# Kernel tuning notes

Measured on AMD Instinct MI355X. Metric: run time of the kernel, lower is better.

The kernel has to match this reference:

```python
import jax, jax.numpy as jnp
import numpy as np

EPS = 1e-6
N_HEADS = 16


def _stable_softmax(x):
    # max subtracted with stop_gradient (torch .detach()), clamp to [-50, 50], eps in denom
    x_max = jax.lax.stop_gradient(jnp.max(x, axis=-1, keepdims=True))
    exp_x = jnp.exp(jnp.clip(x - x_max, -50.0, 50.0))
    return exp_x / (jnp.sum(exp_x, axis=-1, keepdims=True) + EPS)


def setup_inputs() -> dict:
    key = jax.random.key(0)
    k1, k2, k3 = jax.random.split(key, 3)
    B, S, D = 2, 2048, 1024
    x = jax.random.normal(k1, (B, S, D), dtype=jnp.float32)
    Wqkv = jax.random.normal(k2, (3 * D, D), dtype=jnp.float32) * 0.02
    Wout = jax.random.normal(k3, (D, D), dtype=jnp.float32) * (0.02 / np.sqrt(2))
    return {"x": x, "Wqkv": Wqkv, "Wout": Wout}


def reference(x, Wqkv, Wout):
    B, S, D = x.shape
    H = N_HEADS
    Dh = D // H
    scale = 1.0 / np.sqrt(Dh)
    # qkv projection (torch Linear: x @ W.T), split into q,k,v -> (B,H,S,Dh)
    qkv = (x @ Wqkv.T).reshape(B, S, 3, H, Dh)
    qkv = jnp.transpose(qkv, (2, 0, 3, 1, 4))
    q, k, v = qkv[0], qkv[1], qkv[2]
    # chunked attention is mathematically identical to full attention here
    scores = jnp.einsum('bhqd,bhkd->bhqk', q, k) * scale
    attn = _stable_softmax(scores)
    out = jnp.einsum('bhqk,bhkd->bhqd', attn, v)  # (B,H,S,Dh)
    out = jnp.transpose(out, (0, 2, 1, 3)).reshape(B, S, D)
    return out @ Wout.T
```

## Files before the change

kernel.cpp:

```cpp
#include <hip/hip_runtime.h>
#include <hip/hip_bf16.h>
#include <stdint.h>

#define S_LEN   2048
#define D_MODEL 1024
#define NH      16
#define DH      64
#define BATCH   2
#define TOKENS  (BATCH * S_LEN)

typedef __bf16 bf16;
typedef __bf16 bf16x8 __attribute__((ext_vector_type(8)));
typedef __bf16 b16x4  __attribute__((ext_vector_type(4)));
typedef float  f32x4  __attribute__((ext_vector_type(4)));
typedef float  f32x16 __attribute__((ext_vector_type(16)));
typedef unsigned int uint32;

__device__ __forceinline__ void async_lds16(const void* g, void* l) {
  __builtin_amdgcn_global_load_lds((__attribute__((address_space(1))) void*)g,
                                   (__attribute__((address_space(3))) void*)l,
                                   16, 0, 0);
}

__global__ __launch_bounds__(256) void convert2_kernel(
    const float* __restrict__ s0, bf16* __restrict__ d0, int n0,
    const float* __restrict__ s1, bf16* __restrict__ d1, int n1) {
  int i = blockIdx.x * 256 + threadIdx.x;
  const float* s;
  bf16* d;
  if (i < n0) {
    s = s0 + (size_t)i * 8; d = d0 + (size_t)i * 8;
  } else {
    i -= n0;
    if (i >= n1) return;
    s = s1 + (size_t)i * 8; d = d1 + (size_t)i * 8;
  }
  const f32x4 a = *(const f32x4*)s;
  const f32x4 b = *(const f32x4*)(s + 4);
  bf16x8 o;
#pragma unroll
  for (int j = 0; j < 4; j++) { o[j] = (bf16)a[j]; o[j + 4] = (bf16)b[j]; }
  *(bf16x8*)d = o;
}

#define BM 128
#define BN 128
#define BK 32

#define GEMM_CORE(APTR, BPTR, KDIM)                                              \
  __shared__ __align__(16) bf16 As[BM * BK];                                     \
  __shared__ __align__(16) bf16 Bs[BN * BK];                                     \
  const int tid  = threadIdx.x;                                                  \
  const int wave = tid >> 6, lane = tid & 63;                                    \
  const int quad = lane >> 4, l16 = lane & 15;                                   \
  const int m0 = blockIdx.y * BM;                                                \
  const int n0 = blockIdx.x * BN;                                                \
  const int wm = (wave >> 1) * 64, wn = (wave & 1) * 64;                         \
  f32x4 acc[4][4] = {};                                                          \
  const int c0 = tid, c1 = tid + 256;                                            \
  for (int k0 = 0; k0 < (KDIM); k0 += BK) {                                      \
    async_lds16((APTR) + (size_t)(m0 + (c0 >> 2)) * (KDIM) + k0 + (c0 & 3) * 8,  \
                As + c0 * 8);                                                    \
    async_lds16((APTR) + (size_t)(m0 + (c1 >> 2)) * (KDIM) + k0 + (c1 & 3) * 8,  \
                As + c1 * 8);                                                    \
    async_lds16((BPTR) + (size_t)(n0 + (c0 >> 2)) * (KDIM) + k0 + (c0 & 3) * 8,  \
                Bs + c0 * 8);                                                    \
    async_lds16((BPTR) + (size_t)(n0 + (c1 >> 2)) * (KDIM) + k0 + (c1 & 3) * 8,  \
                Bs + c1 * 8);                                                    \
    __syncthreads();                                                             \
    bf16x8 af[4], bfr[4];                                                        \
    _Pragma("unroll") for (int i = 0; i < 4; i++)                                \
        af[i] = *(const bf16x8*)(As + (wm + i * 16 + l16) * BK + quad * 8);      \
    _Pragma("unroll") for (int j = 0; j < 4; j++)                                \
        bfr[j] = *(const bf16x8*)(Bs + (wn + j * 16 + l16) * BK + quad * 8);     \
    _Pragma("unroll") for (int i = 0; i < 4; i++)                                \
      _Pragma("unroll") for (int j = 0; j < 4; j++)                              \
        acc[i][j] = __builtin_amdgcn_mfma_f32_16x16x32_bf16(af[i], bfr[j],       \
                                                            acc[i][j], 0, 0, 0); \
    __syncthreads();                                                             \
  }

__global__ __launch_bounds__(256) void gemm_qkv_kernel(
    const bf16* __restrict__ X, const bf16* __restrict__ W,
    bf16* __restrict__ Qo, bf16* __restrict__ Ko, bf16* __restrict__ VTo) {
  GEMM_CORE(X, W, D_MODEL)
  const int t = n0 >> 10;
#pragma unroll
  for (int i = 0; i < 4; i++) {
    const int rowb = m0 + wm + i * 16 + quad * 4;
    const int b = rowb >> 11, s0 = rowb & 2047;
#pragma unroll
    for (int j = 0; j < 4; j++) {
      const int col = n0 + wn + j * 16 + l16;
      const int h = (col >> 6) & 15, d = col & 63;
      if (t == 2) {
        b16x4 v4;
#pragma unroll
        for (int r = 0; r < 4; r++) v4[r] = (bf16)acc[i][j][r];
        *(b16x4*)(VTo + ((size_t)(b * NH + h) * DH + d) * S_LEN + s0) = v4;
      } else {
#pragma unroll
        for (int r = 0; r < 4; r++) {
          const float v = acc[i][j][r];
          if (t == 0)
            Qo[((size_t)(b * NH + h) * S_LEN + s0 + r) * DH + d] = (bf16)(v * 0.125f);
          else
            Ko[((size_t)(b * NH + h) * S_LEN + s0 + r) * DH + d] = (bf16)v;
        }
      }
    }
  }
}

#define BM2 64
#define BN2 128

__global__ __launch_bounds__(256) void gemm_out_kernel(
    const bf16* __restrict__ A, const bf16* __restrict__ W,
    float* __restrict__ Out) {
  __shared__ __align__(16) bf16 As[BM2 * BK];
  __shared__ __align__(16) bf16 Bs[BN2 * BK];
  const int tid  = threadIdx.x;
  const int wave = tid >> 6, lane = tid & 63;
  const int quad = lane >> 4, l16 = lane & 15;
  const int m0 = blockIdx.y * BM2;
  const int n0 = blockIdx.x * BN2;
  const int wm = (wave >> 1) * 32, wn = (wave & 1) * 64;
  f32x4 acc[2][4] = {};
  const int c0 = tid, c1 = tid + 256;
  for (int k0 = 0; k0 < D_MODEL; k0 += BK) {
    async_lds16(A + (size_t)(m0 + (c0 >> 2)) * D_MODEL + k0 + (c0 & 3) * 8,
                As + c0 * 8);
    async_lds16(W + (size_t)(n0 + (c0 >> 2)) * D_MODEL + k0 + (c0 & 3) * 8,
                Bs + c0 * 8);
    async_lds16(W + (size_t)(n0 + (c1 >> 2)) * D_MODEL + k0 + (c1 & 3) * 8,
                Bs + c1 * 8);
    __syncthreads();
    bf16x8 af[2], bfr[4];
#pragma unroll
    for (int i = 0; i < 2; i++)
      af[i] = *(const bf16x8*)(As + (wm + i * 16 + l16) * BK + quad * 8);
#pragma unroll
    for (int j = 0; j < 4; j++)
      bfr[j] = *(const bf16x8*)(Bs + (wn + j * 16 + l16) * BK + quad * 8);
#pragma unroll
    for (int i = 0; i < 2; i++)
#pragma unroll
      for (int j = 0; j < 4; j++)
        acc[i][j] = __builtin_amdgcn_mfma_f32_16x16x32_bf16(af[i], bfr[j],
                                                            acc[i][j], 0, 0, 0);
    __syncthreads();
  }
#pragma unroll
  for (int i = 0; i < 2; i++) {
    const int rowb = m0 + wm + i * 16 + quad * 4;
#pragma unroll
    for (int j = 0; j < 4; j++) {
      const int col = n0 + wn + j * 16 + l16;
#pragma unroll
      for (int r = 0; r < 4; r++)
        Out[(size_t)(rowb + r) * D_MODEL + col] = acc[i][j][r];
    }
  }
}

__global__ __launch_bounds__(512, 2) void attn_kernel(
    const bf16* __restrict__ Q, const bf16* __restrict__ K,
    const bf16* __restrict__ VT, bf16* __restrict__ AO) {
  __shared__ __align__(16) bf16 smem[2][2][2 * 64 * 64];

  const int tid  = threadIdx.x;
  const int lane = tid & 63;
  const int wave = tid >> 6;
  const int g    = wave >> 2;
  const int qw   = wave & 3;
  const int l31  = lane & 31;
  const int hi   = lane >> 5;
  const int sw   = l31 & 7;

  const int bid = (blockIdx.x & 7) * 32 + (blockIdx.x >> 3);
  const int qb  = bid & 7;
  const int bh  = bid >> 3;

  const bf16* qp = Q  + ((size_t)bh * S_LEN + qb * 256 + qw * 64 + l31) * DH;
  const bf16* kp = K  + (size_t)bh * S_LEN * DH;
  const bf16* vp = VT + (size_t)bh * DH * S_LEN;

  bf16x8 qf0[4], qf1[4];
#pragma unroll
  for (int dk = 0; dk < 4; dk++) {
    qf0[dk] = *(const bf16x8*)(qp + dk * 16 + hi * 8);
    qf1[dk] = *(const bf16x8*)(qp + 32 * DH + dk * 16 + hi * 8);
  }

  const int gtid = tid & 255;
  const int cid0 = gtid, cid1 = gtid + 256;
  const int r0 = cid0 >> 3, c0 = (cid0 & 7) ^ (r0 & 7);
  const int r1 = cid1 >> 3, c1 = (cid1 & 7) ^ (r1 & 7);
  const bf16* ka0 = kp + (size_t)(g * 64 + r0) * DH + c0 * 8;
  const bf16* ka1 = kp + (size_t)(g * 64 + r1) * DH + c1 * 8;
  const bf16* va0 = vp + (size_t)r0 * S_LEN + g * 64 + c0 * 8;
  const bf16* va1 = vp + (size_t)r1 * S_LEN + g * 64 + c1 * 8;
  const int ld0 = cid0 * 8, ld1 = cid1 * 8;

  f32x16 oT0[2] = {}, oT1[2] = {};
  float lsum0 = 0.f, lsum1 = 0.f;

  bf16* sg = &smem[g][0][0];

#define STAGE(B)                                                                 \
  {                                                                              \
    bf16* s = sg + (B) * (2 * 64 * 64);                                          \
    async_lds16(ka0, s + ld0);                                                   \
    async_lds16(ka1, s + ld1);                                                   \
    async_lds16(va0, s + 4096 + ld0);                                            \
    async_lds16(va1, s + 4096 + ld1);                                            \
    ka0 += 8192; ka1 += 8192; va0 += 128; va1 += 128;                            \
  }

  STAGE(0)

#pragma unroll 2
  for (int t = 0; t < 16; t++) {
    const int cur = t & 1;
    asm volatile("s_waitcnt vmcnt(0)" ::: "memory");
    __builtin_amdgcn_s_barrier();
    if (t < 15) {
      STAGE(cur ^ 1)
    }

    const bf16* sb = sg + cur * (2 * 64 * 64);

    bf16x8 vfr[8];
#pragma unroll
    for (int dt = 0; dt < 2; dt++)
#pragma unroll
      for (int ks = 0; ks < 4; ks++)
        vfr[dt * 4 + ks] = *(const bf16x8*)(sb + 4096 + (dt * 32 + l31) * 64 +
                                            (((ks * 2 + hi) ^ sw) * 8));

    f32x16 st0[2] = {}, st1[2] = {};
    __builtin_amdgcn_s_setprio(1);
#pragma unroll
    for (int kt = 0; kt < 2; kt++)
#pragma unroll
      for (int dk = 0; dk < 4; dk++) {
        const bf16x8 kf = *(const bf16x8*)(sb + (kt * 32 + l31) * 64 +
                                           (((dk * 2 + hi) ^ sw) * 8));
        st0[kt] = __builtin_amdgcn_mfma_f32_32x32x16_bf16(kf, qf0[dk], st0[kt], 0, 0, 0);
        st1[kt] = __builtin_amdgcn_mfma_f32_32x32x16_bf16(kf, qf1[dk], st1[kt], 0, 0, 0);
      }
    __builtin_amdgcn_s_setprio(0);

#pragma unroll
    for (int kt = 0; kt < 2; kt++)
#pragma unroll
      for (int hk = 0; hk < 2; hk++) {
        const int ks = kt * 2 + hk;
        float e0[8], e1[8];
#pragma unroll
        for (int r = 0; r < 8; r++) e0[r] = __expf(st0[kt][hk * 8 + r]);
#pragma unroll
        for (int r = 0; r < 8; r++) e1[r] = __expf(st1[kt][hk * 8 + r]);
        lsum0 += ((e0[0] + e0[1]) + (e0[2] + e0[3])) + ((e0[4] + e0[5]) + (e0[6] + e0[7]));
        lsum1 += ((e1[0] + e1[1]) + (e1[2] + e1[3])) + ((e1[4] + e1[5]) + (e1[6] + e1[7]));
        uint32 p00, p01, p02, p03, p10, p11, p12, p13;
        asm("v_cvt_pk_bf16_f32 %0, %1, %2" : "=v"(p00) : "v"(e0[0]), "v"(e0[1]));
        asm("v_cvt_pk_bf16_f32 %0, %1, %2" : "=v"(p01) : "v"(e0[2]), "v"(e0[3]));
        asm("v_cvt_pk_bf16_f32 %0, %1, %2" : "=v"(p02) : "v"(e0[4]), "v"(e0[5]));
        asm("v_cvt_pk_bf16_f32 %0, %1, %2" : "=v"(p03) : "v"(e0[6]), "v"(e0[7]));
        asm("v_cvt_pk_bf16_f32 %0, %1, %2" : "=v"(p10) : "v"(e1[0]), "v"(e1[1]));
        asm("v_cvt_pk_bf16_f32 %0, %1, %2" : "=v"(p11) : "v"(e1[2]), "v"(e1[3]));
        asm("v_cvt_pk_bf16_f32 %0, %1, %2" : "=v"(p12) : "v"(e1[4]), "v"(e1[5]));
        asm("v_cvt_pk_bf16_f32 %0, %1, %2" : "=v"(p13) : "v"(e1[6]), "v"(e1[7]));
        asm("v_permlane32_swap_b32 %0, %1" : "+v"(p00), "+v"(p02));
        asm("v_permlane32_swap_b32 %0, %1" : "+v"(p01), "+v"(p03));
        asm("v_permlane32_swap_b32 %0, %1" : "+v"(p10), "+v"(p12));
        asm("v_permlane32_swap_b32 %0, %1" : "+v"(p11), "+v"(p13));
        union { uint32 u[4]; bf16x8 v; } pf0, pf1;
        pf0.u[0] = p00; pf0.u[1] = p01; pf0.u[2] = p02; pf0.u[3] = p03;
        pf1.u[0] = p10; pf1.u[1] = p11; pf1.u[2] = p12; pf1.u[3] = p13;
        __builtin_amdgcn_s_setprio(1);
#pragma unroll
        for (int dt = 0; dt < 2; dt++) {
          oT0[dt] = __builtin_amdgcn_mfma_f32_32x32x16_bf16(vfr[dt * 4 + ks], pf0.v,
                                                            oT0[dt], 0, 0, 0);
          oT1[dt] = __builtin_amdgcn_mfma_f32_32x32x16_bf16(vfr[dt * 4 + ks], pf1.v,
                                                            oT1[dt], 0, 0, 0);
        }
        __builtin_amdgcn_s_setprio(0);
      }
  }
#undef STAGE

  __syncthreads();

  lsum0 += __shfl_xor(lsum0, 32);
  lsum1 += __shfl_xor(lsum1, 32);

  float* mO = (float*)&smem[0][0][0];
  float* mL = mO + 256 * 32;
  const int mrow = qw * 64 + lane;

  if (g == 1) {
#pragma unroll
    for (int j = 0; j < 8; j++) {
      const int dt = j >> 2, rb = (j & 3) * 4;
      f32x4 c = { oT0[dt][rb], oT0[dt][rb + 1], oT0[dt][rb + 2], oT0[dt][rb + 3] };
      *(f32x4*)((char*)mO + mrow * 128 + ((j ^ (lane & 7)) * 16)) = c;
    }
    mL[mrow] = lsum0;
  }
  __syncthreads();
  if (g == 0) {
#pragma unroll
    for (int j = 0; j < 8; j++) {
      const int dt = j >> 2, rb = (j & 3) * 4;
      const f32x4 c = *(const f32x4*)((char*)mO + mrow * 128 + ((j ^ (lane & 7)) * 16));
#pragma unroll
      for (int rr = 0; rr < 4; rr++) oT0[dt][rb + rr] += c[rr];
    }
    lsum0 += mL[mrow];
  }
  __syncthreads();
  if (g == 1) {
#pragma unroll
    for (int j = 0; j < 8; j++) {
      const int dt = j >> 2, rb = (j & 3) * 4;
      f32x4 c = { oT1[dt][rb], oT1[dt][rb + 1], oT1[dt][rb + 2], oT1[dt][rb + 3] };
      *(f32x4*)((char*)mO + mrow * 128 + ((j ^ (lane & 7)) * 16)) = c;
    }
    mL[mrow] = lsum1;
  }
  __syncthreads();
  if (g == 0) {
#pragma unroll
    for (int j = 0; j < 8; j++) {
      const int dt = j >> 2, rb = (j & 3) * 4;
      const f32x4 c = *(const f32x4*)((char*)mO + mrow * 128 + ((j ^ (lane & 7)) * 16));
#pragma unroll
      for (int rr = 0; rr < 4; rr++) oT1[dt][rb + rr] += c[rr];
    }
    lsum1 += mL[mrow];

    const float inv0 = 1.0f / (lsum0 + 1e-6f);
    const float inv1 = 1.0f / (lsum1 + 1e-6f);
    const int b = bh >> 4, h = bh & 15;
    const int srow = qb * 256 + qw * 64 + l31;
    const size_t base0 = (size_t)(b * S_LEN + srow) * D_MODEL + h * DH;
    const size_t base1 = base0 + (size_t)32 * D_MODEL;
#pragma unroll
    for (int dt = 0; dt < 2; dt++)
#pragma unroll
      for (int rg = 0; rg < 4; rg++) {
        b16x4 o4;
#pragma unroll
        for (int rr = 0; rr < 4; rr++) o4[rr] = (bf16)(oT0[dt][rg * 4 + rr] * inv0);
        *(b16x4*)(AO + base0 + dt * 32 + rg * 8 + hi * 4) = o4;
      }
#pragma unroll
    for (int dt = 0; dt < 2; dt++)
#pragma unroll
      for (int rg = 0; rg < 4; rg++) {
        b16x4 o4;
#pragma unroll
        for (int rr = 0; rr < 4; rr++) o4[rr] = (bf16)(oT1[dt][rg * 4 + rr] * inv1);
        *(b16x4*)(AO + base1 + dt * 32 + rg * 8 + hi * 4) = o4;
      }
  }
}

extern "C" void kernel_launch(void* const* d_in, const int* in_sizes, int n_in,
                              void* d_out, int out_size, void* d_ws, size_t ws_size,
                              hipStream_t stream) {
  const float* x    = (const float*)d_in[0];
  const float* wqkv = (const float*)d_in[1];
  const float* wout = (const float*)d_in[2];
  float* out = (float*)d_out;

  bf16* Q  = (bf16*)d_ws;
  bf16* K  = Q  + (size_t)TOKENS * D_MODEL;
  bf16* VT = K  + (size_t)TOKENS * D_MODEL;
  bf16* xb = VT + (size_t)TOKENS * D_MODEL;
  bf16* AO = xb;
  bf16* wqkvb = (bf16*)d_out;
  bf16* woutb = Q;

  const int nx = TOKENS * D_MODEL / 8;
  const int nw = 3 * D_MODEL * D_MODEL / 8;
  const int no = D_MODEL * D_MODEL / 8;
  convert2_kernel<<<dim3((nx + nw) / 256), dim3(256), 0, stream>>>(
      x, xb, nx, wqkv, wqkvb, nw);

  gemm_qkv_kernel<<<dim3(3 * D_MODEL / BN, TOKENS / BM), dim3(256), 0, stream>>>(
      xb, wqkvb, Q, K, VT);

  attn_kernel<<<dim3(BATCH * NH * (S_LEN / 256)), dim3(512), 0, stream>>>(Q, K, VT, AO);

  convert2_kernel<<<dim3(no / 256), dim3(256), 0, stream>>>(
      wout, woutb, no, wout, woutb, 0);

  gemm_out_kernel<<<dim3(D_MODEL / BN2, TOKENS / BM2), dim3(256), 0, stream>>>(
      AO, woutb, out);
}
```

Measured before the change: 179.8 us.

## Rewrite QKV GEMM with 256x256 tiles, 8 waves and swizzled double-buffered LDS

Replaces the 128x128, 4-wave QKV projection GEMM with a 256x256 tile computed by 8 waves, using a BK of 64. Loads are XOR-swizzled and double-buffered in 128 KB of dynamic LDS. Global-to-LDS copies are split into quarter-tile stages interleaved with MFMA bursts, with barriers and s_setprio raised around the MFMA bursts. The aim is more operand reuse per LDS byte, fewer bank conflicts and overlap of loads with compute. In exchange the grid shrinks to 192 blocks with roughly one block per CU, and the hand-scheduled buffer reuse is delicate.

```diff
diff --git a/kernel.cpp b/kernel.cpp
--- a/kernel.cpp
+++ b/kernel.cpp
@@ -21,6 +21,8 @@
                                    (__attribute__((address_space(3))) void*)l,
                                    16, 0, 0);
 }
+
+#define MFMA16(a, b, c) __builtin_amdgcn_mfma_f32_16x16x32_bf16((a), (b), (c), 0, 0, 0)
 
 __global__ __launch_bounds__(256) void convert2_kernel(
     const float* __restrict__ s0, bf16* __restrict__ d0, int n0,
@@ -43,75 +45,171 @@
   *(bf16x8*)d = o;
 }
 
-#define BM 128
-#define BN 128
-#define BK 32
-
-#define GEMM_CORE(APTR, BPTR, KDIM)                                              \
-  __shared__ __align__(16) bf16 As[BM * BK];                                     \
-  __shared__ __align__(16) bf16 Bs[BN * BK];                                     \
-  const int tid  = threadIdx.x;                                                  \
-  const int wave = tid >> 6, lane = tid & 63;                                    \
-  const int quad = lane >> 4, l16 = lane & 15;                                   \
-  const int m0 = blockIdx.y * BM;                                                \
-  const int n0 = blockIdx.x * BN;                                                \
-  const int wm = (wave >> 1) * 64, wn = (wave & 1) * 64;                         \
-  f32x4 acc[4][4] = {};                                                          \
-  const int c0 = tid, c1 = tid + 256;                                            \
-  for (int k0 = 0; k0 < (KDIM); k0 += BK) {                                      \
-    async_lds16((APTR) + (size_t)(m0 + (c0 >> 2)) * (KDIM) + k0 + (c0 & 3) * 8,  \
-                As + c0 * 8);                                                    \
-    async_lds16((APTR) + (size_t)(m0 + (c1 >> 2)) * (KDIM) + k0 + (c1 & 3) * 8,  \
-                As + c1 * 8);                                                    \
-    async_lds16((BPTR) + (size_t)(n0 + (c0 >> 2)) * (KDIM) + k0 + (c0 & 3) * 8,  \
-                Bs + c0 * 8);                                                    \
-    async_lds16((BPTR) + (size_t)(n0 + (c1 >> 2)) * (KDIM) + k0 + (c1 & 3) * 8,  \
-                Bs + c1 * 8);                                                    \
-    __syncthreads();                                                             \
-    bf16x8 af[4], bfr[4];                                                        \
-    _Pragma("unroll") for (int i = 0; i < 4; i++)                                \
-        af[i] = *(const bf16x8*)(As + (wm + i * 16 + l16) * BK + quad * 8);      \
-    _Pragma("unroll") for (int j = 0; j < 4; j++)                                \
-        bfr[j] = *(const bf16x8*)(Bs + (wn + j * 16 + l16) * BK + quad * 8);     \
-    _Pragma("unroll") for (int i = 0; i < 4; i++)                                \
-      _Pragma("unroll") for (int j = 0; j < 4; j++)                              \
-        acc[i][j] = __builtin_amdgcn_mfma_f32_16x16x32_bf16(af[i], bfr[j],       \
-                                                            acc[i][j], 0, 0, 0); \
-    __syncthreads();                                                             \
-  }
-
-__global__ __launch_bounds__(256) void gemm_qkv_kernel(
+__global__ __launch_bounds__(512, 2) void gemm_qkv_kernel(
     const bf16* __restrict__ X, const bf16* __restrict__ W,
     bf16* __restrict__ Qo, bf16* __restrict__ Ko, bf16* __restrict__ VTo) {
-  GEMM_CORE(X, W, D_MODEL)
-  const int t = n0 >> 10;
-#pragma unroll
-  for (int i = 0; i < 4; i++) {
+  extern __shared__ __align__(16) bf16 smem[];
+  bf16* const Asb = smem;
+  bf16* const Bsb = smem + 32768;
+
+  const int tid  = threadIdx.x;
+  const int wave = tid >> 6, lane = tid & 63;
+  const int quad = lane >> 4, l16 = lane & 15;
+  const int wm = (wave >> 2) * 128;
+  const int wn = (wave & 3) * 64;
+  const int m0 = blockIdx.y * 256;
+  const int n0 = blockIdx.x * 256;
+
+  const int rowc  = tid >> 3;
+  const int koffc = ((tid & 7) ^ (rowc & 7)) * 8;
+  const bf16* pAlo = X + (size_t)(m0 + rowc) * D_MODEL + koffc;
+  const bf16* pAhi = X + (size_t)(m0 + 128 + rowc) * D_MODEL + koffc;
+  const bf16* pBlo = W + (size_t)(n0 + rowc) * D_MODEL + koffc;
+  const bf16* pBhi = W + (size_t)(n0 + 128 + rowc) * D_MODEL + koffc;
+  const int ldc = tid * 8;
+
+  const int swr = l16 & 7;
+  const int ko0 = ((0 + quad) ^ swr) * 8;
+  const int ko1 = ((4 + quad) ^ swr) * 8;
+
+  f32x4 acc[8][4] = {};
+  bf16x8 af[4][2], bfr[4][2];
+
+#define STG(P, LB)                                                        \
+  { async_lds16((P), (LB) + ldc);                                         \
+    async_lds16((P) + (size_t)64 * D_MODEL, (LB) + ldc + 4096); }
+
+#define BAR()                                                             \
+  { asm volatile("" ::: "memory");                                        \
+    __builtin_amdgcn_s_barrier();                                         \
+    asm volatile("" ::: "memory"); }
+
+  STG(pAlo, Asb)                 pAlo += 64;
+  STG(pAhi, Asb + 8192)          pAhi += 64;
+  STG(pBlo, Bsb)                 pBlo += 64;
+  STG(pBhi, Bsb + 8192)          pBhi += 64;
+  STG(pAlo, Asb + 16384)         pAlo += 64;
+  STG(pAhi, Asb + 16384 + 8192)  pAhi += 64;
+  asm volatile("s_waitcnt vmcnt(4)" ::: "memory");
+  __builtin_amdgcn_s_barrier();
+
+#pragma unroll 2
+  for (int t = 0; t < 16; t++) {
+    const int cur = t & 1;
+    const bf16* Ac = Asb + cur * 16384;
+    const bf16* Bc = Bsb + cur * 16384;
+    bf16* An = Asb + cur * 16384;
+    bf16* Bn = Bsb + (cur ^ 1) * 16384;
+
+#pragma unroll
+    for (int i = 0; i < 4; i++) {
+      af[i][0] = *(const bf16x8*)(Ac + (wm + i * 16 + l16) * 64 + ko0);
+      af[i][1] = *(const bf16x8*)(Ac + (wm + i * 16 + l16) * 64 + ko1);
+    }
+#pragma unroll
+    for (int j = 0; j < 2; j++) {
+      bfr[j][0] = *(const bf16x8*)(Bc + (wn + j * 16 + l16) * 64 + ko0);
+      bfr[j][1] = *(const bf16x8*)(Bc + (wn + j * 16 + l16) * 64 + ko1);
+    }
+    if (t < 15) { STG(pBlo, Bn) pBlo += 64; }
+    BAR();
+    __builtin_amdgcn_s_setprio(1);
+#pragma unroll
+    for (int i = 0; i < 4; i++)
+#pragma unroll
+      for (int j = 0; j < 2; j++) {
+        acc[i][j] = MFMA16(af[i][0], bfr[j][0], acc[i][j]);
+        acc[i][j] = MFMA16(af[i][1], bfr[j][1], acc[i][j]);
+      }
+    __builtin_amdgcn_s_setprio(0);
+    BAR();
+
+#pragma unroll
+    for (int j = 2; j < 4; j++) {
+      bfr[j][0] = *(const bf16x8*)(Bc + (wn + j * 16 + l16) * 64 + ko0);
+      bfr[j][1] = *(const bf16x8*)(Bc + (wn + j * 16 + l16) * 64 + ko1);
+    }
+    if (t < 15) { STG(pBhi, Bn + 8192) pBhi += 64; }
+    BAR();
+    __builtin_amdgcn_s_setprio(1);
+#pragma unroll
+    for (int i = 0; i < 4; i++)
+#pragma unroll
+      for (int j = 2; j < 4; j++) {
+        acc[i][j] = MFMA16(af[i][0], bfr[j][0], acc[i][j]);
+        acc[i][j] = MFMA16(af[i][1], bfr[j][1], acc[i][j]);
+      }
+    __builtin_amdgcn_s_setprio(0);
+    BAR();
+
+#pragma unroll
+    for (int i = 0; i < 4; i++) {
+      af[i][0] = *(const bf16x8*)(Ac + (wm + (i + 4) * 16 + l16) * 64 + ko0);
+      af[i][1] = *(const bf16x8*)(Ac + (wm + (i + 4) * 16 + l16) * 64 + ko1);
+    }
+    if (t < 14) { STG(pAlo, An) pAlo += 64; }
+    BAR();
+    __builtin_amdgcn_s_setprio(1);
+#pragma unroll
+    for (int i = 0; i < 4; i++)
+#pragma unroll
+      for (int j = 0; j < 2; j++) {
+        acc[i + 4][j] = MFMA16(af[i][0], bfr[j][0], acc[i + 4][j]);
+        acc[i + 4][j] = MFMA16(af[i][1], bfr[j][1], acc[i + 4][j]);
+      }
+    __builtin_amdgcn_s_setprio(0);
+    BAR();
+
+    if (t < 14) {
+      STG(pAhi, An + 8192) pAhi += 64;
+      asm volatile("s_waitcnt vmcnt(4)" ::: "memory");
+    } else if (t == 14) {
+      asm volatile("s_waitcnt vmcnt(0)" ::: "memory");
+    }
+    BAR();
+    __builtin_amdgcn_s_setprio(1);
+#pragma unroll
+    for (int i = 0; i < 4; i++)
+#pragma unroll
+      for (int j = 2; j < 4; j++) {
+        acc[i + 4][j] = MFMA16(af[i][0], bfr[j][0], acc[i + 4][j]);
+        acc[i + 4][j] = MFMA16(af[i][1], bfr[j][1], acc[i + 4][j]);
+      }
+    __builtin_amdgcn_s_setprio(0);
+    BAR();
+  }
+#undef STG
+#undef BAR
+
+  const int tq = n0 >> 10;
+#pragma unroll
+  for (int i = 0; i < 8; i++) {
     const int rowb = m0 + wm + i * 16 + quad * 4;
-    const int b = rowb >> 11, s0 = rowb & 2047;
+    const int b = rowb >> 11, s0r = rowb & 2047;
 #pragma unroll
     for (int j = 0; j < 4; j++) {
       const int col = n0 + wn + j * 16 + l16;
       const int h = (col >> 6) & 15, d = col & 63;
-      if (t == 2) {
+      if (tq == 2) {
         b16x4 v4;
 #pragma unroll
         for (int r = 0; r < 4; r++) v4[r] = (bf16)acc[i][j][r];
-        *(b16x4*)(VTo + ((size_t)(b * NH + h) * DH + d) * S_LEN + s0) = v4;
+        *(b16x4*)(VTo + ((size_t)(b * NH + h) * DH + d) * S_LEN + s0r) = v4;
       } else {
 #pragma unroll
         for (int r = 0; r < 4; r++) {
           const float v = acc[i][j][r];
-          if (t == 0)
-            Qo[((size_t)(b * NH + h) * S_LEN + s0 + r) * DH + d] = (bf16)(v * 0.125f);
+          if (tq == 0)
+            Qo[((size_t)(b * NH + h) * S_LEN + s0r + r) * DH + d] = (bf16)(v * 0.125f);
           else
-            Ko[((size_t)(b * NH + h) * S_LEN + s0 + r) * DH + d] = (bf16)v;
+            Ko[((size_t)(b * NH + h) * S_LEN + s0r + r) * DH + d] = (bf16)v;
         }
       }
     }
   }
 }
 
+#define BK  32
 #define BM2 64
 #define BN2 128
 
@@ -147,8 +245,7 @@
     for (int i = 0; i < 2; i++)
 #pragma unroll
       for (int j = 0; j < 4; j++)
-        acc[i][j] = __builtin_amdgcn_mfma_f32_16x16x32_bf16(af[i], bfr[j],
-                                                            acc[i][j], 0, 0, 0);
+        acc[i][j] = MFMA16(af[i], bfr[j], acc[i][j]);
     __syncthreads();
   }
 #pragma unroll
@@ -392,8 +489,8 @@
   convert2_kernel<<<dim3((nx + nw) / 256), dim3(256), 0, stream>>>(
       x, xb, nx, wqkv, wqkvb, nw);
 
-  gemm_qkv_kernel<<<dim3(3 * D_MODEL / BN, TOKENS / BM), dim3(256), 0, stream>>>(
-      xb, wqkvb, Q, K, VT);
+  gemm_qkv_kernel<<<dim3(3 * D_MODEL / 256, TOKENS / 256), dim3(512),
+                    131072, stream>>>(xb, wqkvb, Q, K, VT);
 
   attn_kernel<<<dim3(BATCH * NH * (S_LEN / 256)), dim3(512), 0, stream>>>(Q, K, VT, AO);
 
```

After: 177.6 us. About the same (-1.3%).
